# Performance work log

Measured on AMD Instinct MI355X. Metric: run time of the kernel, lower is better.

The kernel has to match this reference:

```python
import jax, jax.numpy as jnp
import numpy as np

N_HEAD, D_MODEL, D_HEAD, D_OUT = 16, 1024, 64, 1024
Q_INNER = N_HEAD * D_HEAD


def setup_inputs() -> dict:
    key = jax.random.key(0)
    ks = jax.random.split(key, 10)
    B, S = 1, 4096
    hidden_state = jax.random.normal(ks[0], (B, S, D_MODEL), dtype=jnp.float32)
    # causal mask, (B,1,S,S), 1 = attend, 0 = masked
    attention_mask = jnp.tril(jnp.ones((S, S), dtype=jnp.int32))[None, None, :, :]
    s = 0.02
    Wq = jax.random.normal(ks[1], (D_MODEL, Q_INNER), dtype=jnp.float32) * s
    bq = jnp.zeros((Q_INNER,), dtype=jnp.float32)
    Wk = jax.random.normal(ks[2], (D_MODEL, D_HEAD), dtype=jnp.float32) * s
    bk = jnp.zeros((D_HEAD,), dtype=jnp.float32)
    Wv = jax.random.normal(ks[3], (D_MODEL, D_HEAD), dtype=jnp.float32) * s
    bv = jnp.zeros((D_HEAD,), dtype=jnp.float32)
    Wo = jax.random.normal(ks[4], (Q_INNER, D_OUT), dtype=jnp.float32) * s
    bo = jnp.zeros((D_OUT,), dtype=jnp.float32)
    return {"hidden_state": hidden_state, "attention_mask": attention_mask,
            "Wq": Wq, "bq": bq, "Wk": Wk, "bk": bk, "Wv": Wv, "bv": bv,
            "Wo": Wo, "bo": bo}


def reference(hidden_state, attention_mask, Wq, bq, Wk, bk, Wv, bv, Wo, bo):
    B, S, _ = hidden_state.shape
    q = hidden_state @ Wq + bq                    # (B,S,H*Dh)
    k = hidden_state @ Wk + bk                    # (B,S,Dh) single shared KV head
    v = hidden_state @ Wv + bv                    # (B,S,Dh)
    q = q.reshape(B, S, N_HEAD, D_HEAD)           # (B,S,H,Dh)
    scale = 1.0 / jnp.sqrt(jnp.float32(D_HEAD))
    # scores: (B,H,S,S) — shared K broadcast over heads
    scores = jnp.einsum('bqhd,bkd->bhqk', q, k) * scale
    scores = jnp.where(attention_mask == 0, -jnp.inf, scores)
    probs = jax.nn.softmax(scores, axis=-1)
    out = jnp.einsum('bhqk,bkd->bqhd', probs, v)  # (B,S,H,Dh)
    out = out.reshape(B, S, Q_INNER)
    return out @ Wo + bo
```

## Files before the change

### kernel.cpp

```cpp
#include <hip/hip_runtime.h>
#include <hip/hip_bf16.h>
#include <math.h>

typedef __bf16 bf16;
typedef __bf16 bf16x4 __attribute__((ext_vector_type(4)));
typedef __bf16 bf16x8 __attribute__((ext_vector_type(8)));
typedef float f32x4 __attribute__((ext_vector_type(4)));

#define AS1(p) ((const __attribute__((address_space(1))) void*)(p))
#define AS3(p) ((__attribute__((address_space(3))) void*)(p))

__device__ __forceinline__ void gld_lds16(const void* g, void* l) {
  __builtin_amdgcn_global_load_lds(AS1(g), AS3(l), 16, 0, 0);
}

#define MFMA16(a, b, c) __builtin_amdgcn_mfma_f32_16x16x32_bf16((a), (b), (c), 0, 0, 0)

#define QSCALE_F 0.180336880f

struct Sched { unsigned short e[768]; };
constexpr Sched make_sched() {
  Sched s{};
  for (int bx = 0; bx < 256; ++bx) {
    int h = bx >> 4, i = bx & 15;
    s.e[bx]       = (unsigned short)(((31 - i) << 6) | (h << 2) | 1);
    s.e[bx + 256] = (unsigned short)(((31 - i) << 6) | (h << 2) | 2);
    s.e[bx + 512] = (unsigned short)((i << 6) | (h << 2) | 0);
  }
  return s;
}
__device__ constexpr Sched SCHED = make_sched();

__global__ void cast_f32_bf16(const float4* __restrict__ in, bf16* __restrict__ out, int n4) {
  int i = blockIdx.x * blockDim.x + threadIdx.x;
  if (i < n4) {
    float4 v = in[i];
    bf16x4 o4 = {(bf16)v.x, (bf16)v.y, (bf16)v.z, (bf16)v.w};
    *(bf16x4*)(out + (size_t)i * 4) = o4;
  }
}

__global__ void prep_wqkv(const float* __restrict__ Wq, const float* __restrict__ Wk,
                          const float* __restrict__ Wv, bf16* __restrict__ out) {
  __shared__ float t[64][65];
  const int ob = blockIdx.y;
  const float* src;
  int C, c0;
  if (ob < 16)      { src = Wq; C = 1024; c0 = ob * 64; }
  else if (ob == 16){ src = Wk; C = 64;   c0 = 0; }
  else              { src = Wv; C = 64;   c0 = 0; }
  const int r0 = blockIdx.x * 64;
  const int tx = threadIdx.x & 63, ty = threadIdx.x >> 6;
#pragma unroll
  for (int j = 0; j < 16; j++)
    t[ty + j * 4][tx] = src[(size_t)(r0 + ty + j * 4) * C + c0 + tx];
  __syncthreads();
#pragma unroll
  for (int j = 0; j < 16; j++)
    out[(size_t)(ob * 64 + ty + j * 4) * 1024 + r0 + tx] = (bf16)t[tx][ty + j * 4];
}

__global__ void transpose_cast_f32_bf16(const float* __restrict__ in, bf16* __restrict__ out,
                                        int C, int ldout) {
  __shared__ float t[64][65];
  int r0 = blockIdx.y * 64, c0 = blockIdx.x * 64;
  int tx = threadIdx.x & 63, ty = threadIdx.x >> 6;
#pragma unroll
  for (int j = 0; j < 16; j++)
    t[ty + j * 4][tx] = in[(size_t)(r0 + ty + j * 4) * C + c0 + tx];
  __syncthreads();
#pragma unroll
  for (int j = 0; j < 16; j++)
    out[(size_t)(c0 + ty + j * 4) * ldout + r0 + tx] = (bf16)t[tx][ty + j * 4];
}

__global__ void pack_bias3(const float* __restrict__ bq, const float* __restrict__ bk,
                           const float* __restrict__ bv, float* __restrict__ o) {
  int i = blockIdx.x * 256 + threadIdx.x;
  if (i < 1024) o[i] = bq[i];
  else if (i < 1088) o[i] = bk[i - 1024];
  else if (i < 1152) o[i] = bv[i - 1088];
}

template <int OUTF32, int QSCALE>
__global__ __launch_bounds__(256) void gemm_bt64(const bf16* __restrict__ A,
                                                 const bf16* __restrict__ B,
                                                 const float* __restrict__ bias,
                                                 void* __restrict__ Cout,
                                                 int M, int N, int K) {
  __shared__ bf16 As[64 * 32];
  __shared__ bf16 Bs[128 * 32];
  const int tid = threadIdx.x, w = tid >> 6, lane = tid & 63;
  const int g = lane >> 4, r = lane & 15;
  const int cpx = gridDim.x >> 3;
  const int l = (blockIdx.x & 7) * cpx + (blockIdx.x >> 3);
  const int ntn = N >> 7;
  const int my = l / ntn, mx = l - my * ntn;
  const int tm = my * 64, tn = mx * 128;
  const int wr = w >> 1, wc = w & 1;

  f32x4 acc[2][4] = {};

  const char* gA = (const char*)(A + (size_t)tm * K);
  const char* gB = (const char*)(B + (size_t)tn * K);
  const int linA = w * 1024 + lane * 16;
  const int lin0 = (w * 2 + 0) * 1024 + lane * 16;
  const int lin1 = (w * 2 + 1) * 1024 + lane * 16;
  const int rA = linA >> 6, cA = linA & 63;
  const int rB0 = lin0 >> 6, cB0 = lin0 & 63;
  const int rB1 = lin1 >> 6, cB1 = lin1 & 63;
  char* ldsA  = (char*)As + w * 1024;
  char* ldsB0 = (char*)Bs + (w * 2 + 0) * 1024;
  char* ldsB1 = (char*)Bs + (w * 2 + 1) * 1024;

  for (int k0 = 0; k0 < K; k0 += 32) {
    gld_lds16(gA + (size_t)rA * (K * 2) + k0 * 2 + cA, ldsA);
    gld_lds16(gB + (size_t)rB0 * (K * 2) + k0 * 2 + cB0, ldsB0);
    gld_lds16(gB + (size_t)rB1 * (K * 2) + k0 * 2 + cB1, ldsB1);
    __syncthreads();

    bf16x8 af[2], bfr[4];
#pragma unroll
    for (int m = 0; m < 2; m++)
      af[m] = *(const bf16x8*)&As[(wr * 32 + m * 16 + r) * 32 + g * 8];
#pragma unroll
    for (int n = 0; n < 4; n++)
      bfr[n] = *(const bf16x8*)&Bs[(wc * 64 + n * 16 + r) * 32 + g * 8];
#pragma unroll
    for (int m = 0; m < 2; m++)
#pragma unroll
      for (int n = 0; n < 4; n++)
        acc[m][n] = MFMA16(af[m], bfr[n], acc[m][n]);
    __syncthreads();
  }

#pragma unroll
  for (int m = 0; m < 2; m++) {
#pragma unroll
    for (int n = 0; n < 4; n++) {
      int crow = tm + wr * 32 + m * 16 + g * 4;
      int ccol = tn + wc * 64 + n * 16 + r;
      float bb = bias[ccol];
      float sc = (QSCALE && ccol < 1024) ? QSCALE_F : 1.0f;
#pragma unroll
      for (int j = 0; j < 4; j++) {
        float v = (acc[m][n][j] + bb) * sc;
        if (OUTF32)
          ((float*)Cout)[(size_t)(crow + j) * N + ccol] = v;
        else
          ((bf16*)Cout)[(size_t)(crow + j) * N + ccol] = (bf16)v;
      }
    }
  }
}

__global__ void kv_prep(const bf16* __restrict__ QKV, bf16* __restrict__ Ksw,
                        bf16* __restrict__ Vtsw) {
  __shared__ bf16 Vld[64][72];
  const int kv0 = blockIdx.x * 64;
  const int tid = threadIdx.x;
#pragma unroll
  for (int cc = 0; cc < 2; cc++) {
    const int c = tid + cc * 256;
    const int kvl = c >> 3, c8 = c & 7;
    bf16x8 kv8 = *(const bf16x8*)(QKV + (size_t)(kv0 + kvl) * 1152 + 1024 + c8 * 8);
    *(bf16x8*)(Ksw + (size_t)(kv0 + kvl) * 64 + ((c8 * 8) ^ ((kvl & 7) << 3))) = kv8;
    bf16x8 vv = *(const bf16x8*)(QKV + (size_t)(kv0 + kvl) * 1152 + 1088 + c8 * 8);
#pragma unroll
    for (int e = 0; e < 8; e++) Vld[c8 * 8 + e][kvl] = vv[e];
  }
  __syncthreads();
#pragma unroll
  for (int cc = 0; cc < 2; cc++) {
    const int c = tid + cc * 256;
    const int d = c >> 3, k8 = c & 7;
    bf16x8 o8 = *(const bf16x8*)&Vld[d][k8 * 8];
    *(bf16x8*)(Vtsw + (size_t)d * 4096 + kv0 + ((k8 * 8) ^ ((d & 7) << 3))) = o8;
  }
}

__global__ __launch_bounds__(256) void mqa_fwd(const bf16* __restrict__ QKV,
                                               const bf16* __restrict__ Ksw,
                                               const bf16* __restrict__ Vtsw,
                                               bf16* __restrict__ AO,
                                               float* __restrict__ po,
                                               float* __restrict__ psum) {
  __shared__ bf16 Ks[2][64 * 64];
  __shared__ bf16 Vs[2][64 * 64];
  __shared__ bf16 Ps[4 * 32 * 64];

  const int e = SCHED.e[blockIdx.x];
  const int qt = e >> 6, h = (e >> 2) & 15, part = e & 3;
  const int tbeg = (part == 2) ? qt + 1 : 0;
  const int tend = (part == 1) ? qt + 1 : 2 * qt + 2;

  const int tid = threadIdx.x, w = tid >> 6, lane = tid & 63;
  const int g = lane >> 4, r = lane & 15;
  const int qw = qt * 128 + w * 32;
  const int qown0 = qw + r;
  const int qown1 = qw + 16 + r;

  const char* Kg = (const char*)Ksw;
  const char* Vg = (const char*)Vtsw;
  char* PsB = (char*)Ps;
  const int lin0 = w * 2048 + lane * 16;
  const int lin1 = lin0 + 1024;
  const int sz = (r & 7) << 4;

  bf16x8 qf0[2], qf1[2];
#pragma unroll
  for (int kk = 0; kk < 2; kk++) {
    qf0[kk] = *(const bf16x8*)&QKV[(size_t)qown0 * 1152 + h * 64 + kk * 32 + g * 8];
    qf1[kk] = *(const bf16x8*)&QKV[(size_t)qown1 * 1152 + h * 64 + kk * 32 + g * 8];
  }

  const bf16 one = (bf16)1.0f;
  const bf16x8 ones = {one, one, one, one, one, one, one, one};

  f32x4 o[2][4] = {};
  f32x4 sums[2] = {};

  auto STAGE = [&](int t, int b) {
    const int kn = t * 64;
    char* kb = (char*)Ks + b * 8192 + w * 2048;
    char* vb = (char*)Vs + b * 8192 + w * 2048;
    gld_lds16(Kg + (size_t)kn * 128 + lin0, kb);
    gld_lds16(Kg + (size_t)kn * 128 + lin1, kb + 1024);
    gld_lds16(Vg + (size_t)(lin0 >> 7) * 8192 + kn * 2 + (lin0 & 127), vb);
    gld_lds16(Vg + (size_t)(lin1 >> 7) * 8192 + kn * 2 + (lin1 & 127), vb + 1024);
  };

  int buf = 0;
  STAGE(tbeg, 0);
  for (int t = tbeg; t < tend; ++t) {
    if (t + 1 < tend) {
      STAGE(t + 1, buf ^ 1);
      asm volatile("s_waitcnt vmcnt(4)" ::: "memory");
    } else {
      asm volatile("s_waitcnt vmcnt(0)" ::: "memory");
    }
    __builtin_amdgcn_sched_barrier(0);
    __builtin_amdgcn_s_barrier();

    const char* kt = (const char*)Ks + buf * 8192;
    const char* vt = (const char*)Vs + buf * 8192;
    const int kv0 = t * 64;

    f32x4 s0[4], s1[4];
    __builtin_amdgcn_s_setprio(1);
#pragma unroll
    for (int n = 0; n < 4; n++) {
      bf16x8 kf0 = *(const bf16x8*)(kt + (n * 16 + r) * 128 + ((g * 16) ^ sz));
      bf16x8 kf1 = *(const bf16x8*)(kt + (n * 16 + r) * 128 + ((64 + g * 16) ^ sz));
      f32x4 z0 = {0.f, 0.f, 0.f, 0.f};
      z0 = MFMA16(kf0, qf0[0], z0);
      z0 = MFMA16(kf1, qf0[1], z0);
      s0[n] = z0;
      f32x4 z1 = {0.f, 0.f, 0.f, 0.f};
      z1 = MFMA16(kf0, qf1[0], z1);
      z1 = MFMA16(kf1, qf1[1], z1);
      s1[n] = z1;
    }
    __builtin_amdgcn_s_setprio(0);

    if (t >= 2 * qt) {
#pragma unroll
      for (int n = 0; n < 4; n++)
#pragma unroll
        for (int jj = 0; jj < 4; jj++) {
          const int kv = kv0 + n * 16 + g * 4 + jj;
          if (kv > qown0) s0[n][jj] = -3.0e38f;
          if (kv > qown1) s1[n][jj] = -3.0e38f;
        }
    }

#pragma unroll
    for (int n = 0; n < 4; n++) {
      bf16x4 pk0, pk1;
#pragma unroll
      for (int jj = 0; jj < 4; jj++) {
        pk0[jj] = (bf16)__builtin_amdgcn_exp2f(s0[n][jj]);
        pk1[jj] = (bf16)__builtin_amdgcn_exp2f(s1[n][jj]);
      }
      *(bf16x4*)(PsB + w * 4096 + r * 128 + ((n * 32 + g * 8) ^ sz)) = pk0;
      *(bf16x4*)(PsB + w * 4096 + (16 + r) * 128 + ((n * 32 + g * 8) ^ sz)) = pk1;
    }

    asm volatile("s_waitcnt lgkmcnt(0)" ::: "memory");
    __builtin_amdgcn_sched_barrier(0);

    bf16x8 pa00 = *(const bf16x8*)(PsB + w * 4096 + r * 128 + ((g * 16) ^ sz));
    bf16x8 pa01 = *(const bf16x8*)(PsB + w * 4096 + r * 128 + ((64 + g * 16) ^ sz));
    bf16x8 pa10 = *(const bf16x8*)(PsB + w * 4096 + (16 + r) * 128 + ((g * 16) ^ sz));
    bf16x8 pa11 = *(const bf16x8*)(PsB + w * 4096 + (16 + r) * 128 + ((64 + g * 16) ^ sz));
    __builtin_amdgcn_s_setprio(1);
    sums[0] = MFMA16(pa00, ones, sums[0]);
    sums[0] = MFMA16(pa01, ones, sums[0]);
    sums[1] = MFMA16(pa10, ones, sums[1]);
    sums[1] = MFMA16(pa11, ones, sums[1]);
#pragma unroll
    for (int n = 0; n < 4; n++) {
      bf16x8 vf0 = *(const bf16x8*)(vt + (n * 16 + r) * 128 + ((g * 16) ^ sz));
      bf16x8 vf1 = *(const bf16x8*)(vt + (n * 16 + r) * 128 + ((64 + g * 16) ^ sz));
      o[0][n] = MFMA16(pa00, vf0, o[0][n]);
      o[0][n] = MFMA16(pa01, vf1, o[0][n]);
      o[1][n] = MFMA16(pa10, vf0, o[1][n]);
      o[1][n] = MFMA16(pa11, vf1, o[1][n]);
    }
    __builtin_amdgcn_s_setprio(0);
    __builtin_amdgcn_s_barrier();
    buf ^= 1;
  }

  if (part == 0) {
#pragma unroll
    for (int H = 0; H < 2; H++)
#pragma unroll
      for (int jj = 0; jj < 4; jj++) {
        const float inv = 1.f / sums[H][jj];
        const int row = qw + H * 16 + g * 4 + jj;
#pragma unroll
        for (int n = 0; n < 4; n++)
          AO[(size_t)row * 1024 + h * 64 + n * 16 + r] = (bf16)(o[H][n][jj] * inv);
      }
  } else {
    const int slot = ((qt - 16) * 16 + h) * 2 + (part - 1);
    float* pb = po + (size_t)slot * 8192;
#pragma unroll
    for (int H = 0; H < 2; H++)
#pragma unroll
      for (int jj = 0; jj < 4; jj++) {
        const int row = w * 32 + H * 16 + g * 4 + jj;
#pragma unroll
        for (int n = 0; n < 4; n++)
          pb[row * 64 + n * 16 + r] = o[H][n][jj];
        if (r == 0) psum[slot * 128 + row] = sums[H][jj];
      }
  }
}

__global__ __launch_bounds__(256) void combine_split(const float* __restrict__ po,
                                                     const float* __restrict__ psum,
                                                     bf16* __restrict__ AO) {
  const int bxx = blockIdx.x;
  const int qt = 16 + (bxx >> 4), h = bxx & 15;
  const float* a  = po + (size_t)bxx * 16384;
  const float* b  = a + 8192;
  const float* sa = psum + bxx * 256;
  const float* sb = sa + 128;
  const int row = threadIdx.x >> 1, c0 = (threadIdx.x & 1) * 32;
  const float inv = 1.f / (sa[row] + sb[row]);
  const float* pa = a + row * 64 + c0;
  const float* pb = b + row * 64 + c0;
  bf16* dst = AO + (size_t)(qt * 128 + row) * 1024 + h * 64 + c0;
#pragma unroll
  for (int i = 0; i < 8; i++) {
    float4 va = ((const float4*)pa)[i];
    float4 vb = ((const float4*)pb)[i];
    bf16x4 o4 = {(bf16)((va.x + vb.x) * inv), (bf16)((va.y + vb.y) * inv),
                 (bf16)((va.z + vb.z) * inv), (bf16)((va.w + vb.w) * inv)};
    ((bf16x4*)dst)[i] = o4;
  }
}

extern "C" void kernel_launch(void* const* d_in, const int* in_sizes, int n_in,
                              void* d_out, int out_size, void* d_ws, size_t ws_size,
                              hipStream_t stream) {
  const float* H  = (const float*)d_in[0];
  const float* Wq = (const float*)d_in[2];
  const float* bq = (const float*)d_in[3];
  const float* Wk = (const float*)d_in[4];
  const float* bk = (const float*)d_in[5];
  const float* Wv = (const float*)d_in[6];
  const float* bv = (const float*)d_in[7];
  const float* Wo = (const float*)d_in[8];
  const float* bo = (const float*)d_in[9];
  float* out = (float*)d_out;

  const int S = 4096, DM = 1024;

  char* p = (char*)d_ws;
  bf16* Hb    = (bf16*)(p);
  bf16* QKV   = (bf16*)(p + 8388608);
  bf16* Wqkvt = (bf16*)(p + 17825792);
  bf16* Wot   = (bf16*)(p + 20185088);
  float* bqkv = (float*)(p + 22282240);
  bf16* Ksw   = (bf16*)(p + 22286848);
  bf16* Vtsw  = (bf16*)(p + 22811136);
  float* po   = (float*)(p + 23335424);
  float* psum = (float*)(p + 40112640);
  bf16* AOb   = Hb;

  cast_f32_bf16<<<(S * DM / 4 + 255) / 256, 256, 0, stream>>>((const float4*)H, Hb, S * DM / 4);
  prep_wqkv<<<dim3(16, 18), 256, 0, stream>>>(Wq, Wk, Wv, Wqkvt);
  transpose_cast_f32_bf16<<<dim3(16, 16), 256, 0, stream>>>(Wo, Wot, 1024, 1024);
  pack_bias3<<<5, 256, 0, stream>>>(bq, bk, bv, bqkv);

  gemm_bt64<0, 1><<<576, 256, 0, stream>>>(Hb, Wqkvt, bqkv, QKV, S, 1152, 1024);

  kv_prep<<<64, 256, 0, stream>>>(QKV, Ksw, Vtsw);

  mqa_fwd<<<768, 256, 0, stream>>>(QKV, Ksw, Vtsw, AOb, po, psum);
  combine_split<<<256, 256, 0, stream>>>(po, psum, AOb);

  gemm_bt64<1, 0><<<512, 256, 0, stream>>>(AOb, Wot, bo, out, S, 1024, 1024);
}
```

Measured before the change: 125.4 us.

## Double-buffer GEMM with K=64 stages and pre-swizzled operands for conflict-free LDS reads

```diff
diff --git a/kernel.cpp b/kernel.cpp
--- a/kernel.cpp
+++ b/kernel.cpp
@@ -17,6 +17,7 @@
 #define MFMA16(a, b, c) __builtin_amdgcn_mfma_f32_16x16x32_bf16((a), (b), (c), 0, 0, 0)
 
 #define QSCALE_F 0.180336880f
+
 
 struct Sched { unsigned short e[768]; };
 constexpr Sched make_sched() {
@@ -31,12 +32,16 @@
 }
 __device__ constexpr Sched SCHED = make_sched();
 
-__global__ void cast_f32_bf16(const float4* __restrict__ in, bf16* __restrict__ out, int n4) {
+__global__ void cast_f32_bf16_sw(const float4* __restrict__ in, bf16* __restrict__ out,
+                                 int n4) {
   int i = blockIdx.x * blockDim.x + threadIdx.x;
   if (i < n4) {
     float4 v = in[i];
     bf16x4 o4 = {(bf16)v.x, (bf16)v.y, (bf16)v.z, (bf16)v.w};
-    *(bf16x4*)(out + (size_t)i * 4) = o4;
+    const int e = i * 4;
+    const int row = e >> 10;
+    const int idx = (e & ~63) | ((e & 63) ^ ((row & 7) << 3));
+    *(bf16x4*)(out + (size_t)idx) = o4;
   }
 }
 
@@ -56,12 +61,14 @@
     t[ty + j * 4][tx] = src[(size_t)(r0 + ty + j * 4) * C + c0 + tx];
   __syncthreads();
 #pragma unroll
-  for (int j = 0; j < 16; j++)
-    out[(size_t)(ob * 64 + ty + j * 4) * 1024 + r0 + tx] = (bf16)t[tx][ty + j * 4];
-}
-
-__global__ void transpose_cast_f32_bf16(const float* __restrict__ in, bf16* __restrict__ out,
-                                        int C, int ldout) {
+  for (int j = 0; j < 16; j++) {
+    const int orow = ob * 64 + ty + j * 4;
+    out[(size_t)orow * 1024 + r0 + (tx ^ ((orow & 7) << 3))] = (bf16)t[tx][ty + j * 4];
+  }
+}
+
+__global__ void transpose_cast_sw(const float* __restrict__ in, bf16* __restrict__ out,
+                                  int C, int ldout) {
   __shared__ float t[64][65];
   int r0 = blockIdx.y * 64, c0 = blockIdx.x * 64;
   int tx = threadIdx.x & 63, ty = threadIdx.x >> 6;
@@ -70,8 +77,10 @@
     t[ty + j * 4][tx] = in[(size_t)(r0 + ty + j * 4) * C + c0 + tx];
   __syncthreads();
 #pragma unroll
-  for (int j = 0; j < 16; j++)
-    out[(size_t)(c0 + ty + j * 4) * ldout + r0 + tx] = (bf16)t[tx][ty + j * 4];
+  for (int j = 0; j < 16; j++) {
+    const int orow = c0 + ty + j * 4;
+    out[(size_t)orow * ldout + r0 + (tx ^ ((orow & 7) << 3))] = (bf16)t[tx][ty + j * 4];
+  }
 }
 
 __global__ void pack_bias3(const float* __restrict__ bq, const float* __restrict__ bk,
@@ -83,13 +92,13 @@
 }
 
 template <int OUTF32, int QSCALE>
-__global__ __launch_bounds__(256) void gemm_bt64(const bf16* __restrict__ A,
-                                                 const bf16* __restrict__ B,
-                                                 const float* __restrict__ bias,
-                                                 void* __restrict__ Cout,
-                                                 int M, int N, int K) {
-  __shared__ bf16 As[64 * 32];
-  __shared__ bf16 Bs[128 * 32];
+__global__ __launch_bounds__(256) void gemm_bt64k(const bf16* __restrict__ A,
+                                                  const bf16* __restrict__ B,
+                                                  const float* __restrict__ bias,
+                                                  void* __restrict__ Cout,
+                                                  int M, int N, int K) {
+  __shared__ bf16 As[2 * 64 * 64];
+  __shared__ bf16 Bs[2 * 128 * 64];
   const int tid = threadIdx.x, w = tid >> 6, lane = tid & 63;
   const int g = lane >> 4, r = lane & 15;
   const int cpx = gridDim.x >> 3;
@@ -98,40 +107,69 @@
   const int my = l / ntn, mx = l - my * ntn;
   const int tm = my * 64, tn = mx * 128;
   const int wr = w >> 1, wc = w & 1;
+  const int sz = (r & 7) << 4;
 
   f32x4 acc[2][4] = {};
 
   const char* gA = (const char*)(A + (size_t)tm * K);
   const char* gB = (const char*)(B + (size_t)tn * K);
-  const int linA = w * 1024 + lane * 16;
-  const int lin0 = (w * 2 + 0) * 1024 + lane * 16;
-  const int lin1 = (w * 2 + 1) * 1024 + lane * 16;
-  const int rA = linA >> 6, cA = linA & 63;
-  const int rB0 = lin0 >> 6, cB0 = lin0 & 63;
-  const int rB1 = lin1 >> 6, cB1 = lin1 & 63;
-  char* ldsA  = (char*)As + w * 1024;
-  char* ldsB0 = (char*)Bs + (w * 2 + 0) * 1024;
-  char* ldsB1 = (char*)Bs + (w * 2 + 1) * 1024;
-
-  for (int k0 = 0; k0 < K; k0 += 32) {
-    gld_lds16(gA + (size_t)rA * (K * 2) + k0 * 2 + cA, ldsA);
-    gld_lds16(gB + (size_t)rB0 * (K * 2) + k0 * 2 + cB0, ldsB0);
-    gld_lds16(gB + (size_t)rB1 * (K * 2) + k0 * 2 + cB1, ldsB1);
-    __syncthreads();
-
-    bf16x8 af[2], bfr[4];
+  const int linA0 = (w * 2 + 0) * 1024 + lane * 16;
+  const int linA1 = (w * 2 + 1) * 1024 + lane * 16;
+  const int linB0 = (w * 4 + 0) * 1024 + lane * 16;
+  const int linB1 = (w * 4 + 1) * 1024 + lane * 16;
+  const int linB2 = (w * 4 + 2) * 1024 + lane * 16;
+  const int linB3 = (w * 4 + 3) * 1024 + lane * 16;
+
+  auto STAGE = [&](int ks, int b) {
+    char* dA = (char*)As + b * 8192 + (w * 2) * 1024;
+    char* dB = (char*)Bs + b * 16384 + (w * 4) * 1024;
+    gld_lds16(gA + (size_t)(linA0 >> 7) * (K * 2) + ks * 128 + (linA0 & 127), dA);
+    gld_lds16(gA + (size_t)(linA1 >> 7) * (K * 2) + ks * 128 + (linA1 & 127), dA + 1024);
+    gld_lds16(gB + (size_t)(linB0 >> 7) * (K * 2) + ks * 128 + (linB0 & 127), dB);
+    gld_lds16(gB + (size_t)(linB1 >> 7) * (K * 2) + ks * 128 + (linB1 & 127), dB + 1024);
+    gld_lds16(gB + (size_t)(linB2 >> 7) * (K * 2) + ks * 128 + (linB2 & 127), dB + 2048);
+    gld_lds16(gB + (size_t)(linB3 >> 7) * (K * 2) + ks * 128 + (linB3 & 127), dB + 3072);
+  };
+
+  const int nk = K >> 6;
+  STAGE(0, 0);
+  int buf = 0;
+  for (int ks = 0; ks < nk; ++ks) {
+    if (ks + 1 < nk) {
+      STAGE(ks + 1, buf ^ 1);
+      asm volatile("s_waitcnt vmcnt(6)" ::: "memory");
+    } else {
+      asm volatile("s_waitcnt vmcnt(0)" ::: "memory");
+    }
+    __builtin_amdgcn_sched_barrier(0);
+    __builtin_amdgcn_s_barrier();
+
+    const char* at = (const char*)As + buf * 8192;
+    const char* bt = (const char*)Bs + buf * 16384;
+    bf16x8 af[2][2], bfr[4][2];
 #pragma unroll
     for (int m = 0; m < 2; m++)
-      af[m] = *(const bf16x8*)&As[(wr * 32 + m * 16 + r) * 32 + g * 8];
+#pragma unroll
+      for (int kk = 0; kk < 2; kk++)
+        af[m][kk] = *(const bf16x8*)(at + (wr * 32 + m * 16 + r) * 128 +
+                                     ((kk * 64 + g * 16) ^ sz));
 #pragma unroll
     for (int n = 0; n < 4; n++)
-      bfr[n] = *(const bf16x8*)&Bs[(wc * 64 + n * 16 + r) * 32 + g * 8];
+#pragma unroll
+      for (int kk = 0; kk < 2; kk++)
+        bfr[n][kk] = *(const bf16x8*)(bt + (wc * 64 + n * 16 + r) * 128 +
+                                      ((kk * 64 + g * 16) ^ sz));
+    __builtin_amdgcn_s_setprio(1);
 #pragma unroll
     for (int m = 0; m < 2; m++)
 #pragma unroll
-      for (int n = 0; n < 4; n++)
-        acc[m][n] = MFMA16(af[m], bfr[n], acc[m][n]);
-    __syncthreads();
+      for (int n = 0; n < 4; n++) {
+        acc[m][n] = MFMA16(af[m][0], bfr[n][0], acc[m][n]);
+        acc[m][n] = MFMA16(af[m][1], bfr[n][1], acc[m][n]);
+      }
+    __builtin_amdgcn_s_setprio(0);
+    __builtin_amdgcn_s_barrier();
+    buf ^= 1;
   }
 
 #pragma unroll
@@ -319,9 +357,11 @@
       for (int jj = 0; jj < 4; jj++) {
         const float inv = 1.f / sums[H][jj];
         const int row = qw + H * 16 + g * 4 + jj;
+        const int key = (row & 7) << 3;
 #pragma unroll
         for (int n = 0; n < 4; n++)
-          AO[(size_t)row * 1024 + h * 64 + n * 16 + r] = (bf16)(o[H][n][jj] * inv);
+          AO[(size_t)row * 1024 + h * 64 + ((n * 16 + r) ^ key)] =
+              (bf16)(o[H][n][jj] * inv);
       }
   } else {
     const int slot = ((qt - 16) * 16 + h) * 2 + (part - 1);
@@ -352,14 +392,16 @@
   const float inv = 1.f / (sa[row] + sb[row]);
   const float* pa = a + row * 64 + c0;
   const float* pb = b + row * 64 + c0;
-  bf16* dst = AO + (size_t)(qt * 128 + row) * 1024 + h * 64 + c0;
+  const int grow = qt * 128 + row;
+  const int key = (grow & 7) << 3;
+  bf16* dst = AO + (size_t)grow * 1024 + h * 64;
 #pragma unroll
   for (int i = 0; i < 8; i++) {
     float4 va = ((const float4*)pa)[i];
     float4 vb = ((const float4*)pb)[i];
     bf16x4 o4 = {(bf16)((va.x + vb.x) * inv), (bf16)((va.y + vb.y) * inv),
                  (bf16)((va.z + vb.z) * inv), (bf16)((va.w + vb.w) * inv)};
-    ((bf16x4*)dst)[i] = o4;
+    *(bf16x4*)(dst + ((c0 + i * 4) ^ key)) = o4;
   }
 }
 
@@ -391,17 +433,18 @@
   float* psum = (float*)(p + 40112640);
   bf16* AOb   = Hb;
 
-  cast_f32_bf16<<<(S * DM / 4 + 255) / 256, 256, 0, stream>>>((const float4*)H, Hb, S * DM / 4);
+  cast_f32_bf16_sw<<<(S * DM / 4 + 255) / 256, 256, 0, stream>>>((const float4*)H, Hb,
+                                                                 S * DM / 4);
   prep_wqkv<<<dim3(16, 18), 256, 0, stream>>>(Wq, Wk, Wv, Wqkvt);
-  transpose_cast_f32_bf16<<<dim3(16, 16), 256, 0, stream>>>(Wo, Wot, 1024, 1024);
+  transpose_cast_sw<<<dim3(16, 16), 256, 0, stream>>>(Wo, Wot, 1024, 1024);
   pack_bias3<<<5, 256, 0, stream>>>(bq, bk, bv, bqkv);
 
-  gemm_bt64<0, 1><<<576, 256, 0, stream>>>(Hb, Wqkvt, bqkv, QKV, S, 1152, 1024);
+  gemm_bt64k<0, 1><<<576, 256, 0, stream>>>(Hb, Wqkvt, bqkv, QKV, S, 1152, 1024);
 
   kv_prep<<<64, 256, 0, stream>>>(QKV, Ksw, Vtsw);
 
   mqa_fwd<<<768, 256, 0, stream>>>(QKV, Ksw, Vtsw, AOb, po, psum);
   combine_split<<<256, 256, 0, stream>>>(po, psum, AOb);
 
-  gemm_bt64<1, 0><<<512, 256, 0, stream>>>(AOb, Wot, bo, out, S, 1024, 1024);
-}
+  gemm_bt64k<1, 0><<<512, 256, 0, stream>>>(AOb, Wot, bo, out, S, 1024, 1024);
+}
```

New measurement: 118.2 us (median of 2 runs). 1.06x faster.
